# Kernel optimization log

Hardware: AMD Instinct MI355X
Metric: run time of the kernel (lower is better)

Reference implementation:

```python
import jax, jax.numpy as jnp
import numpy as np

GRID_SIZE = 4
ORDER = 3
NUM_BASIS = GRID_SIZE + ORDER  # 7
KNOTS = jnp.linspace(-1.0, 1.0, NUM_BASIS + ORDER + 1)  # 11 knots


def _normalise(x):
    # eval-mode with uninitialized running stats: use batch min/max
    min_val = x.min(axis=0)
    max_val = x.max(axis=0)
    width = jnp.maximum(max_val - min_val, 0.01)
    centre = 0.5 * (max_val + min_val)
    scaled = (x - centre) / (0.5 * width)
    return jnp.clip(scaled, -2.0, 2.0)


def _bspline_basis(x):
    # x: (B, I) -> basis: (B, I, NUM_BASIS), de Boor recursion vectorized over i
    xe = x[..., None]  # (B, I, 1)
    idx = jnp.arange(NUM_BASIS)
    left, right = KNOTS[idx], KNOTS[idx + 1]
    basis = ((xe >= left) & (xe < right)).astype(x.dtype)
    last = jnp.where(xe[..., 0] == KNOTS[NUM_BASIS], 1.0, basis[..., -1])
    basis = basis.at[..., -1].set(last)
    for k in range(1, ORDER + 1):
        d1 = KNOTS[idx + k] - KNOTS[idx]
        d2 = KNOTS[idx + k + 1] - KNOTS[idx + 1]
        b_next = jnp.concatenate([basis[..., 1:], jnp.zeros_like(basis[..., :1])], axis=-1)
        t1 = jnp.where(d1 > 0, (xe - KNOTS[idx]) / jnp.where(d1 > 0, d1, 1.0), 0.0) * basis
        t2 = jnp.where(d2 > 0, (KNOTS[idx + k + 1] - xe) / jnp.where(d2 > 0, d2, 1.0), 0.0) * b_next
        basis = t1 + t2
    return basis


def setup_inputs() -> dict:
    key = jax.random.key(0)
    k1, k2, k3 = jax.random.split(key, 3)
    B, I, O = 8192, 256, 256
    x = jax.random.normal(k1, (B, I), dtype=jnp.float32)
    # xavier-uniform base_weight
    bound = float(np.sqrt(6.0 / (I + O)))
    base_weight = jax.random.uniform(k2, (O, I), minval=-bound, maxval=bound, dtype=jnp.float32)
    spline_weight = jnp.ones((O, I), dtype=jnp.float32)
    spline_coeff = 0.001 * jax.random.normal(k3, (O, I, NUM_BASIS), dtype=jnp.float32)
    bias = jnp.zeros((O,), dtype=jnp.float32)
    return {"x": x, "base_weight": base_weight, "spline_weight": spline_weight,
            "spline_coeff": spline_coeff, "bias": bias}


def reference(x, base_weight, spline_weight, spline_coeff, bias):
    x_norm = _normalise(x)                          # (B, I)
    basis = _bspline_basis(x_norm)                  # (B, I, M)
    silu_x = x_norm * jax.nn.sigmoid(x_norm)        # (B, I)
    base_out = silu_x @ base_weight.T               # sum_i silu_i * W_oi -> (B, O)
    coeff_scaled = spline_coeff * spline_weight[..., None]  # (O, I, M)
    spline_out = jnp.einsum('bim,oim->bo', basis, coeff_scaled)
    return base_out + spline_out + bias[None, :]
```

## Files before the change

kernel.cpp:

```cpp
#include <hip/hip_runtime.h>
#include <hip/hip_bf16.h>

#define B_SZ 8192
#define I_SZ 256
#define O_SZ 256
#define KDIM 2048
#define BM 32
#define BN 64
#define BKT 64
#define NT 32
#define NPART 128

typedef __bf16 bf16x8 __attribute__((ext_vector_type(8)));
typedef float f32x4 __attribute__((ext_vector_type(4)));

__global__ __launch_bounds__(256) void minmax_partial(
    const float* __restrict__ x, float* __restrict__ pmin,
    float* __restrict__ pmax) {
  const int cg = threadIdx.x & 63;
  const int rs = threadIdx.x >> 6;
  const int r0 = blockIdx.x * 64;
  const float* p = x + (size_t)(r0 + rs) * I_SZ + cg * 4;
  float4 mn = {1e30f, 1e30f, 1e30f, 1e30f};
  float4 mx = {-1e30f, -1e30f, -1e30f, -1e30f};
#pragma unroll
  for (int k = 0; k < 16; ++k) {
    const float4 v = *reinterpret_cast<const float4*>(p + (size_t)k * 4 * I_SZ);
    mn.x = fminf(mn.x, v.x); mn.y = fminf(mn.y, v.y);
    mn.z = fminf(mn.z, v.z); mn.w = fminf(mn.w, v.w);
    mx.x = fmaxf(mx.x, v.x); mx.y = fmaxf(mx.y, v.y);
    mx.z = fmaxf(mx.z, v.z); mx.w = fmaxf(mx.w, v.w);
  }
  __shared__ float rmn[4][I_SZ], rmx[4][I_SZ];
  *reinterpret_cast<float4*>(&rmn[rs][cg * 4]) = mn;
  *reinterpret_cast<float4*>(&rmx[rs][cg * 4]) = mx;
  __syncthreads();
  if (threadIdx.x < 64) {
    float4 a, b;
    const int c0 = threadIdx.x * 4;
    a.x = fminf(fminf(rmn[0][c0+0], rmn[1][c0+0]), fminf(rmn[2][c0+0], rmn[3][c0+0]));
    a.y = fminf(fminf(rmn[0][c0+1], rmn[1][c0+1]), fminf(rmn[2][c0+1], rmn[3][c0+1]));
    a.z = fminf(fminf(rmn[0][c0+2], rmn[1][c0+2]), fminf(rmn[2][c0+2], rmn[3][c0+2]));
    a.w = fminf(fminf(rmn[0][c0+3], rmn[1][c0+3]), fminf(rmn[2][c0+3], rmn[3][c0+3]));
    b.x = fmaxf(fmaxf(rmx[0][c0+0], rmx[1][c0+0]), fmaxf(rmx[2][c0+0], rmx[3][c0+0]));
    b.y = fmaxf(fmaxf(rmx[0][c0+1], rmx[1][c0+1]), fmaxf(rmx[2][c0+1], rmx[3][c0+1]));
    b.z = fmaxf(fmaxf(rmx[0][c0+2], rmx[1][c0+2]), fmaxf(rmx[2][c0+2], rmx[3][c0+2]));
    b.w = fmaxf(fmaxf(rmx[0][c0+3], rmx[1][c0+3]), fmaxf(rmx[2][c0+3], rmx[3][c0+3]));
    *reinterpret_cast<float4*>(&pmin[blockIdx.x * I_SZ + c0]) = a;
    *reinterpret_cast<float4*>(&pmax[blockIdx.x * I_SZ + c0]) = b;
  }
}

__global__ void pack_W(const float* __restrict__ bw,
                       const float* __restrict__ sw,
                       const float* __restrict__ coeff,
                       __hip_bfloat16* __restrict__ W,
                       const float* __restrict__ pmin,
                       const float* __restrict__ pmax,
                       float* __restrict__ cenrhw) {
  const int idx = blockIdx.x * blockDim.x + threadIdx.x;
  const int i = idx & (I_SZ - 1);
  const int o = idx >> 8;
  const float s = sw[idx];
  union { __hip_bfloat16 h[8]; float4 f4; } u;
#pragma unroll
  for (int m = 0; m < 7; ++m)
    u.h[m] = __float2bfloat16(coeff[(size_t)idx * 7 + m] * s);
  u.h[7] = __float2bfloat16(bw[idx]);
  const size_t off = (size_t)o * KDIM + (size_t)((i ^ (o & 7)) << 3);
  *reinterpret_cast<float4*>(&W[off]) = u.f4;

  if (blockIdx.x == 0) {
    const int c = threadIdx.x;
    float mn = 1e30f, mx = -1e30f;
#pragma unroll 8
    for (int p = 0; p < NPART; ++p) {
      mn = fminf(mn, pmin[p * I_SZ + c]);
      mx = fmaxf(mx, pmax[p * I_SZ + c]);
    }
    const float width = fmaxf(mx - mn, 0.01f);
    const float rhw = 2.0f / width;
    cenrhw[2 * c]     = rhw;
    cenrhw[2 * c + 1] = -0.5f * (mx + mn) * rhw;
  }
}

__device__ __forceinline__ void async16(const __hip_bfloat16* g, __hip_bfloat16* l) {
  __builtin_amdgcn_global_load_lds(
      (const __attribute__((address_space(1))) void*)g,
      (__attribute__((address_space(3))) void*)l, 16, 0, 0);
}

__global__ __launch_bounds__(256, 4) void gemm_fused(
    const float* __restrict__ x, const __hip_bfloat16* __restrict__ W,
    const float* __restrict__ cenrhw, const float* __restrict__ bias,
    float* __restrict__ out) {
  __shared__ __align__(16) __hip_bfloat16 Alds[2][BM * BKT];
  __shared__ __align__(16) __hip_bfloat16 Blds[2][BN * BKT];
  __shared__ float2 scl[I_SZ];

  const int t = threadIdx.x;
  const int lane = t & 63;
  const int wave = t >> 6;
  const int wm = wave >> 1, wn = wave & 1;
  const int fr = lane & 15, fk = lane >> 4;

  const int bid = blockIdx.x;
  const int swz = (bid & 7) * 128 + (bid >> 3);
  const int bm = swz >> 2, bn = swz & 3;
  const int r0 = bm * BM, c0 = bn * BN;

  scl[t] = reinterpret_cast<const float2*>(cenrhw)[t];

  const int arow = t >> 3;
  const int af_  = t & 7;
  const float* xp = x + (size_t)(r0 + arow) * I_SZ + af_;

  const __hip_bfloat16* gb0 = W + (size_t)(c0 + (t >> 3)) * KDIM + (t & 7) * 8;

  f32x4 acc[2] = {{0.f,0.f,0.f,0.f},{0.f,0.f,0.f,0.f}};

  auto stageB = [&](int buf, int kt) {
    const size_t k0 = (size_t)kt * BKT;
    async16(gb0 + k0,                     &Blds[buf][t * 8]);
    async16(gb0 + k0 + (size_t)32 * KDIM, &Blds[buf][2048 + t * 8]);
  };

  auto buildA = [&](int buf, int kt, float xv) {
    const float2 s2 = scl[kt * 8 + af_];
    const float xn = __builtin_fmaf(xv, s2.x, s2.y);
    const float sp = __builtin_fmaf(xn, 5.0f, 5.0f);
    const float c6 = fminf(floorf(sp), 6.0f);
    const int ci = (int)c6;
    const float u = sp - c6;
    const float zm = (sp > 7.0f) ? 0.0f : (1.0f / 6.0f);
    const float u2 = u * u, u3 = u2 * u, t1 = 1.0f - u;
    const float q3 = u3 * zm;
    const float q0 = (t1 * t1) * (t1 * zm);
    float h2 = __builtin_fmaf(-3.0f, u, 3.0f);
    h2 = __builtin_fmaf(h2, u, 3.0f);
    h2 = __builtin_fmaf(h2, u, 1.0f);
    const float q2 = h2 * zm;
    float h1 = __builtin_fmaf(3.0f, u, -6.0f);
    h1 = __builtin_fmaf(h1, u2, 4.0f);
    const float q1 = h1 * zm;
    const float silu = xn * __builtin_amdgcn_rcpf(1.0f + __expf(-xn));
    union { __hip_bfloat16 h[8]; float4 f4; } uu;
#pragma unroll
    for (int j = 0; j < 7; ++j) {
      float v = 0.0f;
      v = (ci == j + 3) ? q0 : v;
      v = (ci == j + 2) ? q1 : v;
      v = (ci == j + 1) ? q2 : v;
      v = (ci == j)     ? q3 : v;
      uu.h[j] = __float2bfloat16(v);
    }
    uu.h[7] = __float2bfloat16(silu);
    const int unit = af_ ^ (arow & 7);
    *reinterpret_cast<float4*>(&Alds[buf][arow * BKT + unit * 8]) = uu.f4;
  };

  auto compute = [&](int buf) {
    bf16x8 af[2], bg[2][2];
#pragma unroll
    for (int kk = 0; kk < 2; ++kk) {
      const int row = wm * 16 + fr;
      const int unit = ((kk << 2) | fk) ^ (row & 7);
      af[kk] = *reinterpret_cast<const bf16x8*>(&Alds[buf][row * BKT + unit * 8]);
    }
#pragma unroll
    for (int n = 0; n < 2; ++n)
#pragma unroll
      for (int kk = 0; kk < 2; ++kk) {
        const int row = wn * 32 + n * 16 + fr;
        const int unit = ((kk << 2) | fk) ^ (row & 7);
        bg[n][kk] = *reinterpret_cast<const bf16x8*>(&Blds[buf][row * BKT + unit * 8]);
      }
#pragma unroll
    for (int kk = 0; kk < 2; ++kk)
#pragma unroll
      for (int n = 0; n < 2; ++n)
        acc[n] = __builtin_amdgcn_mfma_f32_16x16x32_bf16(
            af[kk], bg[n][kk], acc[n], 0, 0, 0);
  };

  const float xv0 = xp[0];
  float xpf = xp[8];
  __syncthreads();
  stageB(0, 0);
  buildA(0, 0, xv0);
  __syncthreads();
  int cur = 0;
  for (int kt = 0; kt < NT - 1; ++kt) {
    stageB(cur ^ 1, kt + 1);
    const float xpf2 = xp[min(kt + 2, NT - 1) * 8];
    buildA(cur ^ 1, kt + 1, xpf);
    compute(cur);
    __syncthreads();
    xpf = xpf2;
    cur ^= 1;
  }
  compute(cur);

#pragma unroll
  for (int n = 0; n < 2; ++n) {
    const int col = c0 + wn * 32 + n * 16 + fr;
    const float bc = bias[col];
#pragma unroll
    for (int r = 0; r < 4; ++r) {
      const int row = r0 + wm * 16 + fk * 4 + r;
      out[(size_t)row * O_SZ + col] = acc[n][r] + bc;
    }
  }
}

extern "C" void kernel_launch(void* const* d_in, const int* in_sizes, int n_in,
                              void* d_out, int out_size, void* d_ws, size_t ws_size,
                              hipStream_t stream) {
  const float* x     = (const float*)d_in[0];
  const float* bw    = (const float*)d_in[1];
  const float* sw    = (const float*)d_in[2];
  const float* coeff = (const float*)d_in[3];
  const float* bias  = (const float*)d_in[4];
  float* out = (float*)d_out;

  char* ws = (char*)d_ws;
  __hip_bfloat16* Wbuf = (__hip_bfloat16*)ws;
  float* pmin   = (float*)(ws + (size_t)O_SZ * KDIM * 2);
  float* pmax   = pmin + NPART * I_SZ;
  float* cenrhw = pmax + NPART * I_SZ;

  minmax_partial<<<NPART, 256, 0, stream>>>(x, pmin, pmax);
  pack_W<<<(O_SZ * I_SZ) / 256, 256, 0, stream>>>(bw, sw, coeff, Wbuf,
                                                  pmin, pmax, cenrhw);
  gemm_fused<<<(B_SZ / BM) * (O_SZ / BN), 256, 0, stream>>>(x, Wbuf, cenrhw,
                                                            bias, out);
}
```

Measured before the change: 44.89 us.

## Materialize B-spline/SiLU activation matrix in separate kernel, use 64x64 GEMM tiles

```diff
diff --git a/kernel.cpp b/kernel.cpp
--- a/kernel.cpp
+++ b/kernel.cpp
@@ -5,10 +5,6 @@
 #define I_SZ 256
 #define O_SZ 256
 #define KDIM 2048
-#define BM 32
-#define BN 64
-#define BKT 64
-#define NT 32
 #define NPART 128
 
 typedef __bf16 bf16x8 __attribute__((ext_vector_type(8)));
@@ -85,19 +81,56 @@
   }
 }
 
+__global__ __launch_bounds__(256) void build_A(
+    const float* __restrict__ x, const float* __restrict__ cenrhw,
+    __hip_bfloat16* __restrict__ A) {
+  const int idx = blockIdx.x * blockDim.x + threadIdx.x;
+  const int i = idx & (I_SZ - 1);
+  const int b = idx >> 8;
+  const float2 s2 = reinterpret_cast<const float2*>(cenrhw)[i];
+  const float xn = __builtin_fmaf(x[idx], s2.x, s2.y);
+  const float sp = __builtin_fmaf(xn, 5.0f, 5.0f);
+  const float c6 = fminf(fmaxf(floorf(sp), 0.0f), 6.0f);
+  const int ci = (int)c6;
+  const float u = sp - c6;
+  const float zm = (sp > 7.0f) ? 0.0f : (1.0f / 6.0f);
+  const float u2 = u * u, u3 = u2 * u, t1 = 1.0f - u;
+  const float q3 = u3 * zm;
+  const float q0 = (t1 * t1) * (t1 * zm);
+  float h2 = __builtin_fmaf(-3.0f, u, 3.0f);
+  h2 = __builtin_fmaf(h2, u, 3.0f);
+  h2 = __builtin_fmaf(h2, u, 1.0f);
+  const float q2 = h2 * zm;
+  float h1 = __builtin_fmaf(3.0f, u, -6.0f);
+  h1 = __builtin_fmaf(h1, u2, 4.0f);
+  const float q1 = h1 * zm;
+  const float silu = xn * __builtin_amdgcn_rcpf(1.0f + __expf(-xn));
+  union { __hip_bfloat16 h[8]; float4 f4; } uu;
+#pragma unroll
+  for (int j = 0; j < 7; ++j) {
+    float v = 0.0f;
+    v = (ci == j + 3) ? q0 : v;
+    v = (ci == j + 2) ? q1 : v;
+    v = (ci == j + 1) ? q2 : v;
+    v = (ci == j)     ? q3 : v;
+    uu.h[j] = __float2bfloat16(v);
+  }
+  uu.h[7] = __float2bfloat16(silu);
+  const size_t off = (size_t)b * KDIM + (size_t)((i ^ (b & 7)) << 3);
+  *reinterpret_cast<float4*>(&A[off]) = uu.f4;
+}
+
 __device__ __forceinline__ void async16(const __hip_bfloat16* g, __hip_bfloat16* l) {
   __builtin_amdgcn_global_load_lds(
       (const __attribute__((address_space(1))) void*)g,
       (__attribute__((address_space(3))) void*)l, 16, 0, 0);
 }
 
-__global__ __launch_bounds__(256, 4) void gemm_fused(
-    const float* __restrict__ x, const __hip_bfloat16* __restrict__ W,
-    const float* __restrict__ cenrhw, const float* __restrict__ bias,
-    float* __restrict__ out) {
-  __shared__ __align__(16) __hip_bfloat16 Alds[2][BM * BKT];
-  __shared__ __align__(16) __hip_bfloat16 Blds[2][BN * BKT];
-  __shared__ float2 scl[I_SZ];
+__global__ __launch_bounds__(256, 2) void gemm_kan(
+    const __hip_bfloat16* __restrict__ A, const __hip_bfloat16* __restrict__ W,
+    const float* __restrict__ bias, float* __restrict__ out) {
+  __shared__ __align__(16) __hip_bfloat16 Alds[2][64 * 64];
+  __shared__ __align__(16) __hip_bfloat16 Blds[2][64 * 64];
 
   const int t = threadIdx.x;
   const int lane = t & 63;
@@ -106,112 +139,77 @@
   const int fr = lane & 15, fk = lane >> 4;
 
   const int bid = blockIdx.x;
-  const int swz = (bid & 7) * 128 + (bid >> 3);
+  const int swz = (bid & 7) * ((int)gridDim.x >> 3) + (bid >> 3);
   const int bm = swz >> 2, bn = swz & 3;
-  const int r0 = bm * BM, c0 = bn * BN;
-
-  scl[t] = reinterpret_cast<const float2*>(cenrhw)[t];
-
-  const int arow = t >> 3;
-  const int af_  = t & 7;
-  const float* xp = x + (size_t)(r0 + arow) * I_SZ + af_;
-
-  const __hip_bfloat16* gb0 = W + (size_t)(c0 + (t >> 3)) * KDIM + (t & 7) * 8;
-
-  f32x4 acc[2] = {{0.f,0.f,0.f,0.f},{0.f,0.f,0.f,0.f}};
-
-  auto stageB = [&](int buf, int kt) {
-    const size_t k0 = (size_t)kt * BKT;
-    async16(gb0 + k0,                     &Blds[buf][t * 8]);
-    async16(gb0 + k0 + (size_t)32 * KDIM, &Blds[buf][2048 + t * 8]);
+  const int rowBase = bm * 64, colBase = bn * 64;
+
+  const int srow = t >> 3, sseg = t & 7;
+  const __hip_bfloat16* ga = A + (size_t)(rowBase + srow) * KDIM + sseg * 8;
+  const __hip_bfloat16* gb = W + (size_t)(colBase + srow) * KDIM + sseg * 8;
+
+  f32x4 acc[2][2] = {{{0.f, 0.f, 0.f, 0.f}, {0.f, 0.f, 0.f, 0.f}},
+                     {{0.f, 0.f, 0.f, 0.f}, {0.f, 0.f, 0.f, 0.f}}};
+
+  auto stage = [&](int buf, int kt) {
+    const size_t k0 = (size_t)kt * 64;
+    async16(ga + k0, &Alds[buf][t * 8]);
+    async16(ga + k0 + (size_t)32 * KDIM, &Alds[buf][2048 + t * 8]);
+    async16(gb + k0, &Blds[buf][t * 8]);
+    async16(gb + k0 + (size_t)32 * KDIM, &Blds[buf][2048 + t * 8]);
   };
 
-  auto buildA = [&](int buf, int kt, float xv) {
-    const float2 s2 = scl[kt * 8 + af_];
-    const float xn = __builtin_fmaf(xv, s2.x, s2.y);
-    const float sp = __builtin_fmaf(xn, 5.0f, 5.0f);
-    const float c6 = fminf(floorf(sp), 6.0f);
-    const int ci = (int)c6;
-    const float u = sp - c6;
-    const float zm = (sp > 7.0f) ? 0.0f : (1.0f / 6.0f);
-    const float u2 = u * u, u3 = u2 * u, t1 = 1.0f - u;
-    const float q3 = u3 * zm;
-    const float q0 = (t1 * t1) * (t1 * zm);
-    float h2 = __builtin_fmaf(-3.0f, u, 3.0f);
-    h2 = __builtin_fmaf(h2, u, 3.0f);
-    h2 = __builtin_fmaf(h2, u, 1.0f);
-    const float q2 = h2 * zm;
-    float h1 = __builtin_fmaf(3.0f, u, -6.0f);
-    h1 = __builtin_fmaf(h1, u2, 4.0f);
-    const float q1 = h1 * zm;
-    const float silu = xn * __builtin_amdgcn_rcpf(1.0f + __expf(-xn));
-    union { __hip_bfloat16 h[8]; float4 f4; } uu;
-#pragma unroll
-    for (int j = 0; j < 7; ++j) {
-      float v = 0.0f;
-      v = (ci == j + 3) ? q0 : v;
-      v = (ci == j + 2) ? q1 : v;
-      v = (ci == j + 1) ? q2 : v;
-      v = (ci == j)     ? q3 : v;
-      uu.h[j] = __float2bfloat16(v);
-    }
-    uu.h[7] = __float2bfloat16(silu);
-    const int unit = af_ ^ (arow & 7);
-    *reinterpret_cast<float4*>(&Alds[buf][arow * BKT + unit * 8]) = uu.f4;
-  };
-
   auto compute = [&](int buf) {
-    bf16x8 af[2], bg[2][2];
-#pragma unroll
-    for (int kk = 0; kk < 2; ++kk) {
-      const int row = wm * 16 + fr;
-      const int unit = ((kk << 2) | fk) ^ (row & 7);
-      af[kk] = *reinterpret_cast<const bf16x8*>(&Alds[buf][row * BKT + unit * 8]);
-    }
+    bf16x8 af[2][2], bg[2][2];
+#pragma unroll
+    for (int m = 0; m < 2; ++m)
+#pragma unroll
+      for (int kk = 0; kk < 2; ++kk) {
+        const int row = wm * 32 + m * 16 + fr;
+        const int eo = row * 64 + ((((kk << 2) | fk) ^ (row & 7)) << 3);
+        af[m][kk] = *reinterpret_cast<const bf16x8*>(&Alds[buf][eo]);
+      }
 #pragma unroll
     for (int n = 0; n < 2; ++n)
 #pragma unroll
       for (int kk = 0; kk < 2; ++kk) {
         const int row = wn * 32 + n * 16 + fr;
-        const int unit = ((kk << 2) | fk) ^ (row & 7);
-        bg[n][kk] = *reinterpret_cast<const bf16x8*>(&Blds[buf][row * BKT + unit * 8]);
+        const int eo = row * 64 + ((((kk << 2) | fk) ^ (row & 7)) << 3);
+        bg[n][kk] = *reinterpret_cast<const bf16x8*>(&Blds[buf][eo]);
       }
 #pragma unroll
     for (int kk = 0; kk < 2; ++kk)
 #pragma unroll
-      for (int n = 0; n < 2; ++n)
-        acc[n] = __builtin_amdgcn_mfma_f32_16x16x32_bf16(
-            af[kk], bg[n][kk], acc[n], 0, 0, 0);
+      for (int m = 0; m < 2; ++m)
+#pragma unroll
+        for (int n = 0; n < 2; ++n)
+          acc[m][n] = __builtin_amdgcn_mfma_f32_16x16x32_bf16(
+              af[m][kk], bg[n][kk], acc[m][n], 0, 0, 0);
   };
 
-  const float xv0 = xp[0];
-  float xpf = xp[8];
-  __syncthreads();
-  stageB(0, 0);
-  buildA(0, 0, xv0);
+  stage(0, 0);
   __syncthreads();
   int cur = 0;
+  const int NT = KDIM / 64;
   for (int kt = 0; kt < NT - 1; ++kt) {
-    stageB(cur ^ 1, kt + 1);
-    const float xpf2 = xp[min(kt + 2, NT - 1) * 8];
-    buildA(cur ^ 1, kt + 1, xpf);
+    stage(cur ^ 1, kt + 1);
     compute(cur);
     __syncthreads();
-    xpf = xpf2;
     cur ^= 1;
   }
   compute(cur);
 
 #pragma unroll
-  for (int n = 0; n < 2; ++n) {
-    const int col = c0 + wn * 32 + n * 16 + fr;
-    const float bc = bias[col];
-#pragma unroll
-    for (int r = 0; r < 4; ++r) {
-      const int row = r0 + wm * 16 + fk * 4 + r;
-      out[(size_t)row * O_SZ + col] = acc[n][r] + bc;
+  for (int m = 0; m < 2; ++m)
+#pragma unroll
+    for (int n = 0; n < 2; ++n) {
+      const int col = colBase + wn * 32 + n * 16 + fr;
+      const float bc = bias[col];
+#pragma unroll
+      for (int r = 0; r < 4; ++r) {
+        const int row = rowBase + wm * 32 + m * 16 + fk * 4 + r;
+        out[(size_t)row * O_SZ + col] = acc[m][n][r] + bc;
+      }
     }
-  }
 }
 
 extern "C" void kernel_launch(void* const* d_in, const int* in_sizes, int n_in,
@@ -225,14 +223,15 @@
   float* out = (float*)d_out;
 
   char* ws = (char*)d_ws;
-  __hip_bfloat16* Wbuf = (__hip_bfloat16*)ws;
-  float* pmin   = (float*)(ws + (size_t)O_SZ * KDIM * 2);
+  __hip_bfloat16* Abuf = (__hip_bfloat16*)ws;
+  __hip_bfloat16* Wbuf = (__hip_bfloat16*)(ws + (size_t)B_SZ * KDIM * 2);
+  float* pmin   = (float*)(ws + (size_t)B_SZ * KDIM * 2 + (size_t)O_SZ * KDIM * 2);
   float* pmax   = pmin + NPART * I_SZ;
   float* cenrhw = pmax + NPART * I_SZ;
 
   minmax_partial<<<NPART, 256, 0, stream>>>(x, pmin, pmax);
   pack_W<<<(O_SZ * I_SZ) / 256, 256, 0, stream>>>(bw, sw, coeff, Wbuf,
                                                   pmin, pmax, cenrhw);
-  gemm_fused<<<(B_SZ / BM) * (O_SZ / BN), 256, 0, stream>>>(x, Wbuf, cenrhw,
-                                                            bias, out);
-}
+  build_A<<<(B_SZ * I_SZ) / 256, 256, 0, stream>>>(x, cenrhw, Abuf);
+  gemm_kan<<<(B_SZ / 64) * (O_SZ / 64), 256, 0, stream>>>(Abuf, Wbuf, bias, out);
+}
```

New measurement: 53.52 us. 19.2% more time.
